# Kernel optimization log

Hardware: AMD Instinct MI355X
Metric: run time of the kernel (lower is better)

## Reference

```python
import jax, jax.numpy as jnp
import numpy as np

EPS = 1e-15        # norm / denominator clamp (matches geoopt min_norm)
BALL_EPS = 1e-5    # projection margin: max radius = (1-BALL_EPS)/sqrt(c)
TANH_ARG_MAX = 15.0  # pre-expmap tangent clip so tanh arg stays finite
ATANH_MAX = 1.0 - 1e-7

def _norm(x):
    return jnp.maximum(jnp.linalg.norm(x, axis=-1, keepdims=True), EPS)

def pre_clip(x, c):
    # clip tangent norm so sqrt(c)*||x|| <= TANH_ARG_MAX before expmap0
    maxn = TANH_ARG_MAX / jnp.sqrt(c)
    n = _norm(x)
    return x * jnp.minimum(1.0, maxn / n)

def post_clip(x, c):
    # project onto the open Poincare ball of curvature c
    maxn = (1.0 - BALL_EPS) / jnp.sqrt(c)
    n = _norm(x)
    return x * jnp.minimum(1.0, maxn / n)

def expmap0(u, c):
    sc = jnp.sqrt(c)
    n = _norm(u)
    return jnp.tanh(sc * n) * u / (sc * n)

def logmap0(y, c):
    sc = jnp.sqrt(c)
    n = _norm(y)
    return jnp.arctanh(jnp.minimum(sc * n, ATANH_MAX)) * y / (sc * n)

def mobius_add(x, y, c):
    x2 = jnp.sum(x * x, axis=-1, keepdims=True)
    y2 = jnp.sum(y * y, axis=-1, keepdims=True)
    xy = jnp.sum(x * y, axis=-1, keepdims=True)
    num = (1.0 + 2.0 * c * xy + c * y2) * x + (1.0 - c * x2) * y
    den = 1.0 + 2.0 * c * xy + (c * c) * x2 * y2
    return num / jnp.maximum(den, EPS)

def mobius_scalar_mul(r, x, c):
    sc = jnp.sqrt(c)
    n = _norm(x)
    return jnp.tanh(r * jnp.arctanh(jnp.minimum(sc * n, ATANH_MAX))) * x / (sc * n)


def setup_inputs() -> dict:
    key = jax.random.key(0)
    kx, ky = jax.random.split(key)
    B, N, D = 64, 577, 768
    # scale so points land well inside the ball after expmap0
    x = jax.random.normal(kx, (B, N, D), dtype=jnp.float32) * 0.05
    y = jax.random.normal(ky, (B, N, D), dtype=jnp.float32) * 0.05
    return {
        "x": x,
        "y": y,
        "curv_hra": jnp.asarray(np.log(np.e - 1.0), dtype=jnp.float32),  # inv_softplus(1.0)
        "gamma_raw": jnp.asarray(0.5, dtype=jnp.float32),
        "gamma_scale": jnp.asarray(0.0, dtype=jnp.float32),
        "scale_center": jnp.asarray(0.0, dtype=jnp.float32),
    }


def reference(x, y, curv_hra, gamma_raw, gamma_scale, scale_center):
    c = jax.nn.softplus(curv_hra)  # ball curvature from raw param
    hr_x = post_clip(expmap0(pre_clip(x, c), c), c)
    hr_y = post_clip(expmap0(pre_clip(y, c), c), c)
    s = jax.nn.sigmoid(scale_center)
    g_max = 1.0 + jax.nn.softplus(gamma_scale)
    gamma = g_max * jnp.tanh(gamma_raw)
    # learned Mobius midpoint p between hr_x and hr_y
    sx = post_clip(mobius_scalar_mul(s, hr_x, c), c)
    sy = post_clip(mobius_scalar_mul(1.0 - s, hr_y, c), c)
    p = post_clip(mobius_add(sx, sy, c), c)
    # recenter at p, scale residual branch, add, move back, log to tangent
    x_p = post_clip(mobius_add(-p, hr_x, c), c)
    y_p = post_clip(mobius_add(-p, hr_y, c), c)
    y_s = post_clip(mobius_scalar_mul(gamma, y_p, c), c)
    hres_p = post_clip(mobius_add(x_p, y_s, c), c)
    hres = mobius_add(p, hres_p, c)
    r = post_clip(hres, c)
    return logmap0(r, c)
```

## Files before the change

### kernel.cpp

```cpp
#include <hip/hip_runtime.h>
#include <math.h>

#define F_EPS 1e-15f
#define F_BALL 0.99999f
#define F_TANH_ARG_MAX 15.0f
#define F_ATANH_MAX (1.0f - 1e-7f)
#define F_LOG2E 1.4426950408889634f
#define F_LN2   0.6931471805599453f

__device__ __forceinline__ float rcp_fast(float x) {
    float r = __builtin_amdgcn_rcpf(x);
    return r * (2.0f - x * r);
}
__device__ __forceinline__ float sqrt_fast(float x) { return __builtin_amdgcn_sqrtf(x); }
__device__ __forceinline__ float exp2_fast(float x) { return __builtin_amdgcn_exp2f(x); }
__device__ __forceinline__ float log2_fast(float x) { return __builtin_amdgcn_logf(x); }
__device__ __forceinline__ float exp_fast(float x)  { return exp2_fast(x * F_LOG2E); }

__device__ __forceinline__ float tanh_fast(float x) {
    float ax = fabsf(x);
    float t  = exp2_fast(ax * (-2.0f * F_LOG2E));
    float r  = (1.0f - t) * rcp_fast(1.0f + t);
    return copysignf(r, x);
}
__device__ __forceinline__ float atanh_fast(float z) {
    return (0.5f * F_LN2) * log2_fast((1.0f + z) * rcp_fast(1.0f - z));
}
__device__ __forceinline__ float softplus_fast(float x) {
    return F_LN2 * log2_fast(1.0f + exp2_fast(x * F_LOG2E));
}

struct GramS { float X2, Y2, XY; };
struct ChainP { float c, sc, rcp_sc, maxn_pre, maxn_post, s, gamma; };

__device__ __forceinline__ float gnorm2(const GramS& g, float a, float b) {
    return fmaxf(a * a * g.X2 + 2.0f * a * b * g.XY + b * b * g.Y2, 0.0f);
}
__device__ __forceinline__ float gdot(const GramS& g, float au, float bu, float av, float bv) {
    return au * av * g.X2 + (au * bv + bu * av) * g.XY + bu * bv * g.Y2;
}

__device__ __forceinline__ void madd_c(float c, float u2, float v2, float uv,
                                       float au, float bu, float av, float bv,
                                       float& ao, float& bo) {
    float twocuv = 2.0f * c * uv;
    float A = 1.0f + twocuv + c * v2;
    float B = 1.0f - c * u2;
    float rden = rcp_fast(fmaxf(1.0f + twocuv + c * c * u2 * v2, F_EPS));
    ao = (A * au + B * av) * rden;
    bo = (A * bu + B * bv) * rden;
}

__device__ __forceinline__ float pclip(const GramS& g, float maxn_post, float& a, float& b) {
    float n = fmaxf(sqrt_fast(gnorm2(g, a, b)), F_EPS);
    float s = fminf(1.0f, maxn_post * rcp_fast(n));
    a *= s; b *= s;
    return s * n;
}

__device__ __forceinline__ float msm_coef(float sc, float rcp_sc, float r,
                                          float n_in, float& n_out) {
    float ne = fmaxf(n_in, F_EPS);
    float z  = fminf(sc * ne, F_ATANH_MAX);
    float w  = tanh_fast(r * atanh_fast(z));
    float m  = w * rcp_fast(sc * ne);
    float aw = fabsf(w);
    float s  = fminf(1.0f, F_BALL * rcp_fast(fmaxf(aw, F_EPS)));
    n_out = s * aw * rcp_sc;
    return m * s;
}

__device__ __forceinline__ float hr_c(float nx, float sc, float rcp_sc,
                                      float maxn_pre, float& n_out) {
    float s1 = fminf(1.0f, maxn_pre * rcp_fast(nx));
    float n1 = fmaxf(s1 * nx, F_EPS);
    float t  = tanh_fast(sc * n1);
    float f1 = t * rcp_fast(sc * n1);
    float s2 = fminf(1.0f, F_BALL * rcp_fast(fmaxf(t, F_EPS)));
    n_out = s2 * t * rcp_sc;
    return s1 * f1 * s2;
}

__device__ __forceinline__ void chain_row(float gX2, float gY2, float gXY,
                                          const ChainP& P, float& fa, float& fb) {
    GramS g; g.X2 = gX2; g.Y2 = gY2; g.XY = gXY;
    const float c = P.c, sc = P.sc, rcp_sc = P.rcp_sc;
    const float maxn_pre = P.maxn_pre, maxn_post = P.maxn_post;

    const float nx = fmaxf(sqrt_fast(gX2), F_EPS);
    const float ny = fmaxf(sqrt_fast(gY2), F_EPS);

    float n_hx, n_hy;
    const float hx = hr_c(nx, sc, rcp_sc, maxn_pre, n_hx);
    const float hy = hr_c(ny, sc, rcp_sc, maxn_pre, n_hy);

    float n_sx, n_sy;
    const float sxa = hx * msm_coef(sc, rcp_sc, P.s,        n_hx, n_sx);
    const float syb = hy * msm_coef(sc, rcp_sc, 1.0f - P.s, n_hy, n_sy);

    float pa, pb;
    {
        float u2 = n_sx * n_sx, v2 = n_sy * n_sy;
        float uv = sxa * syb * gXY;
        madd_c(c, u2, v2, uv, sxa, 0.0f, 0.0f, syb, pa, pb);
    }
    const float n_p = pclip(g, maxn_post, pa, pb);
    const float np2 = n_p * n_p;

    float xpa, xpb;
    {
        float v2 = n_hx * n_hx;
        float uv = -hx * (pa * gX2 + pb * gXY);
        madd_c(c, np2, v2, uv, -pa, -pb, hx, 0.0f, xpa, xpb);
    }
    const float n_xp = pclip(g, maxn_post, xpa, xpb);

    float ypa, ypb;
    {
        float v2 = n_hy * n_hy;
        float uv = -hy * (pa * gXY + pb * gY2);
        madd_c(c, np2, v2, uv, -pa, -pb, 0.0f, hy, ypa, ypb);
    }
    float n_yp = pclip(g, maxn_post, ypa, ypb);

    float n_ys;
    {
        float m = msm_coef(sc, rcp_sc, P.gamma, n_yp, n_ys);
        ypa *= m; ypb *= m;
    }

    float ha, hb;
    {
        float u2 = n_xp * n_xp, v2 = n_ys * n_ys;
        float uv = gdot(g, xpa, xpb, ypa, ypb);
        madd_c(c, u2, v2, uv, xpa, xpb, ypa, ypb, ha, hb);
    }
    const float n_h = pclip(g, maxn_post, ha, hb);

    float ra, rb;
    {
        float u2 = np2, v2 = n_h * n_h;
        float uv = gdot(g, pa, pb, ha, hb);
        madd_c(c, u2, v2, uv, pa, pb, ha, hb, ra, rb);
    }
    const float n_r = pclip(g, maxn_post, ra, rb);

    const float nrr = fmaxf(n_r, F_EPS);
    const float z   = fminf(sc * nrr, F_ATANH_MAX);
    const float f   = atanh_fast(z) * rcp_fast(sc * nrr);
    fa = f * ra;
    fb = f * rb;
}

__global__ __launch_bounds__(256, 6) void hra_fused(
    const float* __restrict__ x, const float* __restrict__ y,
    const float* __restrict__ p_curv, const float* __restrict__ p_graw,
    const float* __restrict__ p_gscale, const float* __restrict__ p_scent,
    float* __restrict__ out, int rows)
{
    const int lane = threadIdx.x & 63;
    const int w    = (blockIdx.x << 2) | (threadIdx.x >> 6);
    const int nw   = gridDim.x << 2;

    ChainP P;
    P.c         = softplus_fast(p_curv[0]);
    P.sc        = sqrt_fast(P.c);
    P.rcp_sc    = rcp_fast(P.sc);
    P.maxn_pre  = F_TANH_ARG_MAX * P.rcp_sc;
    P.maxn_post = F_BALL * P.rcp_sc;
    P.s         = rcp_fast(1.0f + exp_fast(-p_scent[0]));
    P.gamma     = (1.0f + softplus_fast(p_gscale[0])) * tanh_fast(p_graw[0]);

    for (int row = w; row < rows; row += nw) {
        const float4* xr = (const float4*)(x + (size_t)row * 768) + lane;
        const float4* yr = (const float4*)(y + (size_t)row * 768) + lane;

        float4 x0 = xr[0],   y0 = yr[0];
        float4 x1 = xr[64],  y1 = yr[64];
        float4 x2 = xr[128], y2 = yr[128];

        float sxx = x0.x*x0.x + x0.y*x0.y + x0.z*x0.z + x0.w*x0.w
                  + x1.x*x1.x + x1.y*x1.y + x1.z*x1.z + x1.w*x1.w
                  + x2.x*x2.x + x2.y*x2.y + x2.z*x2.z + x2.w*x2.w;
        float syy = y0.x*y0.x + y0.y*y0.y + y0.z*y0.z + y0.w*y0.w
                  + y1.x*y1.x + y1.y*y1.y + y1.z*y1.z + y1.w*y1.w
                  + y2.x*y2.x + y2.y*y2.y + y2.z*y2.z + y2.w*y2.w;
        float sxy = x0.x*y0.x + x0.y*y0.y + x0.z*y0.z + x0.w*y0.w
                  + x1.x*y1.x + x1.y*y1.y + x1.z*y1.z + x1.w*y1.w
                  + x2.x*y2.x + x2.y*y2.y + x2.z*y2.z + x2.w*y2.w;

#pragma unroll
        for (int o = 32; o > 0; o >>= 1) {
            sxx += __shfl_xor(sxx, o, 64);
            syy += __shfl_xor(syy, o, 64);
            sxy += __shfl_xor(sxy, o, 64);
        }

        float fa, fb;
        chain_row(sxx, syy, sxy, P, fa, fb);

        const float4* xr2 = xr;
        const float4* yr2 = yr;
        asm volatile("" : "+v"(xr2));
        asm volatile("" : "+v"(yr2));
        float4* outr = (float4*)(out + (size_t)row * 768) + lane;
#pragma unroll
        for (int j = 0; j < 3; ++j) {
            const float4 a = xr2[64 * j];
            const float4 b = yr2[64 * j];
            float4 o;
            o.x = fa * a.x + fb * b.x;
            o.y = fa * a.y + fb * b.y;
            o.z = fa * a.z + fb * b.z;
            o.w = fa * a.w + fb * b.w;
            outr[64 * j] = o;
        }
    }
}

extern "C" void kernel_launch(void* const* d_in, const int* in_sizes, int n_in,
                              void* d_out, int out_size, void* d_ws, size_t ws_size,
                              hipStream_t stream) {
    const float* x = (const float*)d_in[0];
    const float* y = (const float*)d_in[1];
    const float* curv = (const float*)d_in[2];
    const float* graw = (const float*)d_in[3];
    const float* gscale = (const float*)d_in[4];
    const float* scent = (const float*)d_in[5];
    float* out = (float*)d_out;

    const int rows = in_sizes[0] / 768;
    int blocks = (rows + 3) / 4;
    if (blocks > 2048) blocks = 2048;

    hipLaunchKernelGGL(hra_fused, dim3(blocks), dim3(256), 0, stream,
                       x, y, curv, graw, gscale, scent, out, rows);
}
```

Measured before the change: 284.8 us.

## Double-buffer row loads in registers and drop second global read of x,y

Each wave now prefetches the next row's x and y into a second register buffer while it computes the current row, ping-ponging between two buffers. The output is formed from the registers that are already loaded, so x and y are no longer re-read from global memory (the old code relied on cache hits for that second read). The occupancy hint in launch_bounds is removed. Holding up to 48 extra floats per lane raises register pressure, which can lower occupancy.

```diff
diff --git a/kernel.cpp b/kernel.cpp
--- a/kernel.cpp
+++ b/kernel.cpp
@@ -152,7 +152,53 @@
     fb = f * rb;
 }
 
-__global__ __launch_bounds__(256, 6) void hra_fused(
+__device__ __forceinline__ void load_row(const float* __restrict__ x,
+                                         const float* __restrict__ y,
+                                         int row, int lane,
+                                         float4 (&xv)[3], float4 (&yv)[3]) {
+    const float4* xr = (const float4*)(x + (size_t)row * 768) + lane;
+    const float4* yr = (const float4*)(y + (size_t)row * 768) + lane;
+    xv[0] = xr[0];  xv[1] = xr[64];  xv[2] = xr[128];
+    yv[0] = yr[0];  yv[1] = yr[64];  yv[2] = yr[128];
+}
+
+__device__ __forceinline__ void process_row(float4 (&xv)[3], float4 (&yv)[3],
+                                            int row, int lane, const ChainP& P,
+                                            float* __restrict__ out) {
+    float sxx = 0.0f, syy = 0.0f, sxy = 0.0f;
+#pragma unroll
+    for (int j = 0; j < 3; ++j) {
+        sxx += xv[j].x * xv[j].x + xv[j].y * xv[j].y
+             + xv[j].z * xv[j].z + xv[j].w * xv[j].w;
+        syy += yv[j].x * yv[j].x + yv[j].y * yv[j].y
+             + yv[j].z * yv[j].z + yv[j].w * yv[j].w;
+        sxy += xv[j].x * yv[j].x + xv[j].y * yv[j].y
+             + xv[j].z * yv[j].z + xv[j].w * yv[j].w;
+    }
+
+#pragma unroll
+    for (int o = 32; o > 0; o >>= 1) {
+        sxx += __shfl_xor(sxx, o, 64);
+        syy += __shfl_xor(syy, o, 64);
+        sxy += __shfl_xor(sxy, o, 64);
+    }
+
+    float fa, fb;
+    chain_row(sxx, syy, sxy, P, fa, fb);
+
+    float4* outr = (float4*)(out + (size_t)row * 768) + lane;
+#pragma unroll
+    for (int j = 0; j < 3; ++j) {
+        float4 o;
+        o.x = fa * xv[j].x + fb * yv[j].x;
+        o.y = fa * xv[j].y + fb * yv[j].y;
+        o.z = fa * xv[j].z + fb * yv[j].z;
+        o.w = fa * xv[j].w + fb * yv[j].w;
+        outr[64 * j] = o;
+    }
+}
+
+__global__ __launch_bounds__(256) void hra_fused(
     const float* __restrict__ x, const float* __restrict__ y,
     const float* __restrict__ p_curv, const float* __restrict__ p_graw,
     const float* __restrict__ p_gscale, const float* __restrict__ p_scent,
@@ -161,6 +207,7 @@
     const int lane = threadIdx.x & 63;
     const int w    = (blockIdx.x << 2) | (threadIdx.x >> 6);
     const int nw   = gridDim.x << 2;
+    if (w >= rows) return;
 
     ChainP P;
     P.c         = softplus_fast(p_curv[0]);
@@ -171,49 +218,27 @@
     P.s         = rcp_fast(1.0f + exp_fast(-p_scent[0]));
     P.gamma     = (1.0f + softplus_fast(p_gscale[0])) * tanh_fast(p_graw[0]);
 
-    for (int row = w; row < rows; row += nw) {
-        const float4* xr = (const float4*)(x + (size_t)row * 768) + lane;
-        const float4* yr = (const float4*)(y + (size_t)row * 768) + lane;
-
-        float4 x0 = xr[0],   y0 = yr[0];
-        float4 x1 = xr[64],  y1 = yr[64];
-        float4 x2 = xr[128], y2 = yr[128];
-
-        float sxx = x0.x*x0.x + x0.y*x0.y + x0.z*x0.z + x0.w*x0.w
-                  + x1.x*x1.x + x1.y*x1.y + x1.z*x1.z + x1.w*x1.w
-                  + x2.x*x2.x + x2.y*x2.y + x2.z*x2.z + x2.w*x2.w;
-        float syy = y0.x*y0.x + y0.y*y0.y + y0.z*y0.z + y0.w*y0.w
-                  + y1.x*y1.x + y1.y*y1.y + y1.z*y1.z + y1.w*y1.w
-                  + y2.x*y2.x + y2.y*y2.y + y2.z*y2.z + y2.w*y2.w;
-        float sxy = x0.x*y0.x + x0.y*y0.y + x0.z*y0.z + x0.w*y0.w
-                  + x1.x*y1.x + x1.y*y1.y + x1.z*y1.z + x1.w*y1.w
-                  + x2.x*y2.x + x2.y*y2.y + x2.z*y2.z + x2.w*y2.w;
-
-#pragma unroll
-        for (int o = 32; o > 0; o >>= 1) {
-            sxx += __shfl_xor(sxx, o, 64);
-            syy += __shfl_xor(syy, o, 64);
-            sxy += __shfl_xor(sxy, o, 64);
-        }
-
-        float fa, fb;
-        chain_row(sxx, syy, sxy, P, fa, fb);
-
-        const float4* xr2 = xr;
-        const float4* yr2 = yr;
-        asm volatile("" : "+v"(xr2));
-        asm volatile("" : "+v"(yr2));
-        float4* outr = (float4*)(out + (size_t)row * 768) + lane;
-#pragma unroll
-        for (int j = 0; j < 3; ++j) {
-            const float4 a = xr2[64 * j];
-            const float4 b = yr2[64 * j];
-            float4 o;
-            o.x = fa * a.x + fb * b.x;
-            o.y = fa * a.y + fb * b.y;
-            o.z = fa * a.z + fb * b.z;
-            o.w = fa * a.w + fb * b.w;
-            outr[64 * j] = o;
+    float4 xA[3], yA[3], xB[3], yB[3];
+
+    int row = w;
+    load_row(x, y, row, lane, xA, yA);
+    while (true) {
+        const int rowB = row + nw;
+        if (rowB < rows) {
+            load_row(x, y, rowB, lane, xB, yB);
+            process_row(xA, yA, row, lane, P, out);
+            const int rowA2 = rowB + nw;
+            if (rowA2 < rows) {
+                load_row(x, y, rowA2, lane, xA, yA);
+                process_row(xB, yB, rowB, lane, P, out);
+                row = rowA2;
+            } else {
+                process_row(xB, yB, rowB, lane, P, out);
+                return;
+            }
+        } else {
+            process_row(xA, yA, row, lane, P, out);
+            return;
         }
     }
 }
```

Measured after the change: 279.7 us. About the same (-1.8%).
